# Optimization experiments

Hardware: AMD Instinct MI355X
Metric: run time of the kernel (lower is better)

## Reference

```python
import jax, jax.numpy as jnp
import numpy as np

D_MODEL = 1024
N_HEADS = 16
D_K = D_MODEL // N_HEADS


def _xavier(key, shape):
    fan_in, fan_out = shape[1], shape[0]
    a = np.sqrt(6.0 / (fan_in + fan_out))
    return jax.random.uniform(key, shape, jnp.float32, -a, a)


def setup_inputs() -> dict:
    key = jax.random.key(0)
    kx, kq, kk, kv, ko = jax.random.split(key, 5)
    x = jax.random.normal(kx, (2, 2048, D_MODEL), jnp.float32)
    # nn.Linear weights are [out, in]; y = x @ W.T
    Wq = _xavier(kq, (D_MODEL, D_MODEL))
    Wk = _xavier(kk, (D_MODEL, D_MODEL))
    Wv = _xavier(kv, (D_MODEL, D_MODEL))
    Wo = _xavier(ko, (D_MODEL, D_MODEL))
    bo = jnp.zeros((D_MODEL,), jnp.float32)
    return {"x": x, "Wq": Wq, "Wk": Wk, "Wv": Wv, "Wo": Wo, "bo": bo}


def reference(x, Wq, Wk, Wv, Wo, bo):
    B, S, D = x.shape
    def split_heads(t):
        # [B,S,D] -> [B,H,S,d_k]
        return t.reshape(B, S, N_HEADS, D_K).transpose(0, 2, 1, 3)
    Q = split_heads(x @ Wq.T)
    K = split_heads(x @ Wk.T)
    V = split_heads(x @ Wv.T)
    scale = 1.0 / jnp.sqrt(jnp.asarray(D_K, x.dtype))
    scores = jnp.einsum('bhqd,bhkd->bhqk', Q, K) * scale  # [B,H,S,S]
    attn = jax.nn.softmax(scores, axis=-1)
    out = jnp.einsum('bhqk,bhkd->bhqd', attn, V)  # [B,H,S,d_k]
    out = out.transpose(0, 2, 1, 3).reshape(B, S, D)  # merge heads
    return out @ Wo.T + bo
```

## Files before the change

kernel.cpp:

```cpp
#include <hip/hip_runtime.h>


typedef __attribute__((ext_vector_type(8))) short bf16x8;
typedef __attribute__((ext_vector_type(4))) short bf16x4;
typedef __attribute__((ext_vector_type(4))) float f32x4;
typedef __attribute__((ext_vector_type(2))) unsigned int u32x2;
typedef __attribute__((ext_vector_type(4))) unsigned int u32x4;

#define GK 1024
#define SEQ 2048
#define NHEAD 16
#define DKD 64
#define PADW 72

#define MFMA32(a, b, c) __builtin_amdgcn_mfma_f32_16x16x32_bf16((a), (b), (c), 0, 0, 0)

#if __has_builtin(__builtin_amdgcn_exp2f)
#define EXP2(x) __builtin_amdgcn_exp2f(x)
#else
#define EXP2(x) exp2f(x)
#endif

#define QSCALE 0.18033688011f

static __device__ __forceinline__ unsigned short f2bf(float f) {
    unsigned int u = __float_as_uint(f);
    u += 0x7fffu + ((u >> 16) & 1u);
    return (unsigned short)(u >> 16);
}

static __device__ __forceinline__ unsigned int pack_bf2(float a, float b) {
    unsigned int ua = __float_as_uint(a) + 0x8000u;
    unsigned int ub = __float_as_uint(b) + 0x8000u;
    return __builtin_amdgcn_perm(ub, ua, 0x07060302u);
}

__global__ __launch_bounds__(256) void cast_all(const float* __restrict__ x,
                                                const float* __restrict__ wq,
                                                const float* __restrict__ wk,
                                                const float* __restrict__ wv,
                                                const float* __restrict__ wo,
                                                unsigned short* __restrict__ Xb,
                                                unsigned short* __restrict__ Wqkv,
                                                unsigned short* __restrict__ Wob) {
    const int bid = blockIdx.x;
    const float* src; unsigned short* dst; int off;
    if (bid < 4096)      { src = x;  dst = Xb;             off = bid; }
    else if (bid < 5120) { src = wq; dst = Wqkv;           off = bid - 4096; }
    else if (bid < 6144) { src = wk; dst = Wqkv + 1048576; off = bid - 5120; }
    else if (bid < 7168) { src = wv; dst = Wqkv + 2097152; off = bid - 6144; }
    else                 { src = wo; dst = Wob;            off = bid - 7168; }
    const int i = off * 1024 + threadIdx.x * 4;
    float4 v = *(const float4*)(src + i);
    u32x2 p; p.x = pack_bf2(v.x, v.y); p.y = pack_bf2(v.z, v.w);
    *(u32x2*)(dst + i) = p;
}

template <int MODE, int BN>
__global__ __launch_bounds__(256) void gemm_bt(const unsigned short* __restrict__ A,
                                               const unsigned short* __restrict__ Bw,
                                               unsigned short* __restrict__ outb,
                                               float* __restrict__ outf,
                                               const float* __restrict__ bias) {
    constexpr int NJ = BN / 32;
    constexpr int TILE = (128 + BN) * 32;
    constexpr int LOOP_BYTES = 2 * TILE * 2;
    constexpr int EPI_BYTES  = 4 * 64 * PADW * 2;
    constexpr int SMEM_BYTES = (MODE == 0)
        ? (LOOP_BYTES > EPI_BYTES ? LOOP_BYTES : EPI_BYTES)
        : LOOP_BYTES;
    __shared__ __align__(16) unsigned char SMEM[SMEM_BYTES];
    unsigned short* Buf0 = (unsigned short*)SMEM;
    unsigned short* Buf1 = Buf0 + TILE;

    const int t    = threadIdx.x;
    const int lane = t & 63;
    const int w    = t >> 6;
    const int wm   = (w >> 1) * 64;
    const int wn   = (w & 1) * (BN / 2);
    const int bm0  = blockIdx.x * 128;
    const int bn0  = blockIdx.y * BN;
    const int lm   = lane & 15;
    const int lq   = lane >> 4;
    const int swz  = (lq ^ (lm & 3)) * 8;

    const unsigned short* Ab = A + (size_t)bm0 * GK;
    const unsigned short* Bb = Bw + (size_t)bn0 * GK;

    f32x4 acc[4][NJ];
    const f32x4 Z4 = {0.f, 0.f, 0.f, 0.f};
#pragma unroll
    for (int i = 0; i < 4; i++)
#pragma unroll
        for (int j = 0; j < NJ; j++) acc[i][j] = Z4;

    const int q_uni = (t & ~63);

    auto STAGE = [&](unsigned short* Bp, int k0) {
#pragma unroll
        for (int i = 0; i < 2; ++i) {
            int q  = i * 256 + t;
            int r  = q >> 2;
            int gc = (q & 3) ^ (r & 3);
            int q0 = i * 256 + q_uni;
            __builtin_amdgcn_global_load_lds(
                (const __attribute__((address_space(1))) void*)(Ab + (size_t)r * GK + k0 + gc * 8),
                (__attribute__((address_space(3))) void*)(Bp + (size_t)q0 * 8),
                16, 0, 0);
        }
#pragma unroll
        for (int i = 0; i < BN / 64; ++i) {
            int q  = i * 256 + t;
            int r  = q >> 2;
            int gc = (q & 3) ^ (r & 3);
            int q0 = i * 256 + q_uni;
            __builtin_amdgcn_global_load_lds(
                (const __attribute__((address_space(1))) void*)(Bb + (size_t)r * GK + k0 + gc * 8),
                (__attribute__((address_space(3))) void*)(Bp + 128 * 32 + (size_t)q0 * 8),
                16, 0, 0);
        }
    };

    STAGE(Buf0, 0);
    for (int ks = 0; ks < GK / 32; ++ks) {
        __syncthreads();
        unsigned short* Cur = (ks & 1) ? Buf1 : Buf0;
        unsigned short* Nxt = (ks & 1) ? Buf0 : Buf1;
        if (ks + 1 < GK / 32) STAGE(Nxt, (ks + 1) * 32);

        bf16x8 af[4], bf[NJ];
#pragma unroll
        for (int i = 0; i < 4; i++)
            af[i] = *(const bf16x8*)(Cur + (wm + i * 16 + lm) * 32 + swz);
#pragma unroll
        for (int j = 0; j < NJ; j++)
            bf[j] = *(const bf16x8*)(Cur + 128 * 32 + (wn + j * 16 + lm) * 32 + swz);
#pragma unroll
        for (int i = 0; i < 4; i++)
#pragma unroll
            for (int j = 0; j < NJ; j++)
                acc[i][j] = MFMA32(af[i], bf[j], acc[i][j]);
    }

    if (MODE == 0) {
        __syncthreads();
        unsigned short* E  = (unsigned short*)SMEM;
        unsigned short* Ew = E + w * (64 * PADW);
        const int nbase = bn0 + wn;
        const int which = nbase >> 10;
        const int hh    = (nbase & 1023) >> 6;
        const int lq4   = lq * 4;
        if (which != 2) {
            const float sc = (which == 0) ? QSCALE : 1.0f;
#pragma unroll
            for (int i = 0; i < 4; i++)
#pragma unroll
                for (int j = 0; j < 4; j++)
#pragma unroll
                    for (int r = 0; r < 4; r++)
                        Ew[(i * 16 + lq4 + r) * PADW + j * 16 + lm] =
                            f2bf(acc[i][j][r] * sc);
            unsigned short* dst = outb + (size_t)which * 4194304;
#pragma unroll
            for (int rep = 0; rep < 8; ++rep) {
                const int mm = rep * 8 + (lane >> 3);
                const int d0 = (lane & 7) * 8;
                uint4 v = *(const uint4*)(Ew + mm * PADW + d0);
                const int m_g = bm0 + wm + mm;
                const int b = m_g >> 11, s = m_g & 2047;
                *(uint4*)(dst + (((size_t)(b * NHEAD + hh)) * SEQ + s) * DKD + d0) = v;
            }
        } else {
#pragma unroll
            for (int i = 0; i < 4; i++)
#pragma unroll
                for (int j = 0; j < 4; j++) {
                    u32x2 pk;
                    pk.x = pack_bf2(acc[i][j][0], acc[i][j][1]);
                    pk.y = pack_bf2(acc[i][j][2], acc[i][j][3]);
                    *(u32x2*)(Ew + (j * 16 + lm) * PADW + i * 16 + lq4) = pk;
                }
            unsigned short* dst = outb + (size_t)2 * 4194304;
#pragma unroll
            for (int rep = 0; rep < 8; ++rep) {
                const int nn = rep * 8 + (lane >> 3);
                const int mc = (lane & 7) * 8;
                uint4 v = *(const uint4*)(Ew + nn * PADW + mc);
                const int m_g = bm0 + wm + mc;
                const int b = m_g >> 11, s0 = m_g & 2047;
                *(uint4*)(dst + (((size_t)(b * NHEAD + hh)) * DKD + nn) * SEQ + s0) = v;
            }
        }
    } else {
#pragma unroll
        for (int i = 0; i < 4; i++) {
            const int mbase = bm0 + wm + i * 16 + lq * 4;
#pragma unroll
            for (int j = 0; j < NJ; j++) {
                const int n = bn0 + wn + j * 16 + lm;
#pragma unroll
                for (int r = 0; r < 4; r++)
                    outf[(size_t)(mbase + r) * 1024 + n] = acc[i][j][r] + bias[n];
            }
        }
    }
}

__global__ __launch_bounds__(256, 2) void attn_kernel(const unsigned short* __restrict__ Qg,
                                                      const unsigned short* __restrict__ Kg,
                                                      const unsigned short* __restrict__ Vtg,
                                                      unsigned short* __restrict__ Og) {
    __shared__ __align__(16) unsigned short KV[2][2][64 * PADW];

    const int id  = blockIdx.x;
    const int xcd = id & 7;
    const int j8  = id >> 3;
    const int bh  = xcd * 4 + (j8 & 3);
    const int qb  = j8 >> 2;
    const unsigned short* Qp  = Qg  + ((size_t)bh * SEQ + qb * 128) * DKD;
    const unsigned short* Kp  = Kg  + (size_t)bh * SEQ * DKD;
    const unsigned short* Vtp = Vtg + (size_t)bh * DKD * SEQ;

    const int t    = threadIdx.x;
    const int lane = t & 63;
    const int w    = t >> 6;
    const int qg   = w >> 1;
    const int kg   = w & 1;
    const int lm   = lane & 15;
    const int kq   = lane >> 4;

    const f32x4 Z4 = {0.f, 0.f, 0.f, 0.f};

    bf16x8 aq[2][2][2];
#pragma unroll
    for (int h2 = 0; h2 < 2; ++h2)
#pragma unroll
        for (int c = 0; c < 2; ++c)
#pragma unroll
            for (int kk = 0; kk < 2; ++kk)
                aq[h2][c][kk] = *(const bf16x8*)(Qp + (size_t)(h2 * 64 + qg * 32 + c * 16 + lm) * DKD + kk * 32 + kq * 8);

    f32x4 o[2][2][4];
    float ls[2][2];
#pragma unroll
    for (int h2 = 0; h2 < 2; ++h2)
#pragma unroll
        for (int c = 0; c < 2; ++c) {
            ls[h2][c] = 0.f;
#pragma unroll
            for (int dj = 0; dj < 4; ++dj) o[h2][c][dj] = Z4;
        }

    const int sr = t >> 2, sc = (t & 3) * 16;
    uint4 kreg0, kreg1, vreg0, vreg1;
    {
        const unsigned short* kp = Kp + (size_t)sr * DKD + sc;
        const unsigned short* vp = Vtp + (size_t)sr * SEQ + sc;
        uint4 a0 = *(const uint4*)(kp), a1 = *(const uint4*)(kp + 8);
        uint4 b0 = *(const uint4*)(vp), b1 = *(const uint4*)(vp + 8);
        uint4* dk = (uint4*)(&KV[0][0][sr * PADW + sc]); dk[0] = a0; dk[1] = a1;
        uint4* dv = (uint4*)(&KV[0][1][sr * PADW + sc]); dv[0] = b0; dv[1] = b1;
    }
    {
        const unsigned short* kp = Kp + (size_t)(64 + sr) * DKD + sc;
        kreg0 = *(const uint4*)(kp); kreg1 = *(const uint4*)(kp + 8);
        const unsigned short* vp = Vtp + (size_t)sr * SEQ + 64 + sc;
        vreg0 = *(const uint4*)(vp); vreg1 = *(const uint4*)(vp + 8);
    }

    for (int kt = 0; kt < 32; ++kt) {
        asm volatile("s_waitcnt lgkmcnt(0)\n\ts_barrier" ::: "memory");
        const unsigned short* Kc = &KV[kt & 1][0][0];
        const unsigned short* Vc = &KV[kt & 1][1][0];

        bf16x8 ak[2][2];
#pragma unroll
        for (int kc = 0; kc < 2; ++kc)
#pragma unroll
            for (int kk = 0; kk < 2; ++kk)
                ak[kc][kk] = *(const bf16x8*)(Kc + (kg * 32 + kc * 16 + lm) * PADW + kk * 32 + kq * 8);

        if (kt + 1 < 32) {
            uint4* dk = (uint4*)(&KV[(kt + 1) & 1][0][sr * PADW + sc]);
            dk[0] = kreg0; dk[1] = kreg1;
            uint4* dv = (uint4*)(&KV[(kt + 1) & 1][1][sr * PADW + sc]);
            dv[0] = vreg0; dv[1] = vreg1;
        }
        if (kt + 2 < 32) {
            const unsigned short* kp = Kp + (size_t)((kt + 2) * 64 + sr) * DKD + sc;
            kreg0 = *(const uint4*)(kp); kreg1 = *(const uint4*)(kp + 8);
            const unsigned short* vp = Vtp + (size_t)sr * SEQ + (kt + 2) * 64 + sc;
            vreg0 = *(const uint4*)(vp); vreg1 = *(const uint4*)(vp + 8);
        }

        bf16x8 bv[4];
#pragma unroll
        for (int dj = 0; dj < 4; ++dj) {
            const unsigned short* vr = Vc + (dj * 16 + lm) * PADW + kg * 32;
            u32x2 lo = __builtin_bit_cast(u32x2, *(const bf16x4*)(vr + kq * 4));
            u32x2 hi = __builtin_bit_cast(u32x2, *(const bf16x4*)(vr + 16 + kq * 4));
            u32x4 uu; uu.x = lo.x; uu.y = lo.y; uu.z = hi.x; uu.w = hi.y;
            bv[dj] = __builtin_bit_cast(bf16x8, uu);
        }

#pragma unroll
        for (int h2 = 0; h2 < 2; ++h2) {
            f32x4 s[2][2];
            __builtin_amdgcn_s_setprio(1);
#pragma unroll
            for (int kc = 0; kc < 2; ++kc)
#pragma unroll
                for (int c = 0; c < 2; ++c) {
                    s[kc][c] = MFMA32(ak[kc][0], aq[h2][c][0], Z4);
                    s[kc][c] = MFMA32(ak[kc][1], aq[h2][c][1], s[kc][c]);
                }
            __builtin_amdgcn_s_setprio(0);

#pragma unroll
            for (int c = 0; c < 2; ++c) {
#pragma unroll
                for (int kc = 0; kc < 2; ++kc)
#pragma unroll
                    for (int r = 0; r < 4; ++r) s[kc][c][r] = EXP2(s[kc][c][r]);
                ls[h2][c] += ((s[0][c][0] + s[0][c][1]) + (s[0][c][2] + s[0][c][3]))
                           + ((s[1][c][0] + s[1][c][1]) + (s[1][c][2] + s[1][c][3]));
            }

            bf16x8 pa[2];
#pragma unroll
            for (int c = 0; c < 2; ++c) {
                u32x4 uu;
                uu.x = pack_bf2(s[0][c][0], s[0][c][1]);
                uu.y = pack_bf2(s[0][c][2], s[0][c][3]);
                uu.z = pack_bf2(s[1][c][0], s[1][c][1]);
                uu.w = pack_bf2(s[1][c][2], s[1][c][3]);
                pa[c] = __builtin_bit_cast(bf16x8, uu);
            }

            __builtin_amdgcn_s_setprio(1);
#pragma unroll
            for (int dj = 0; dj < 4; ++dj)
#pragma unroll
                for (int c = 0; c < 2; ++c)
                    o[h2][c][dj] = MFMA32(pa[c], bv[dj], o[h2][c][dj]);
            __builtin_amdgcn_s_setprio(0);
        }
    }

    __syncthreads();
    float* Lf = (float*)(&KV[0][0][0]);

#pragma unroll
    for (int h2 = 0; h2 < 2; ++h2)
#pragma unroll
        for (int c = 0; c < 2; ++c) {
            float v = ls[h2][c];
            v += __shfl_xor(v, 16);
            v += __shfl_xor(v, 32);
            if (kq == 0) Lf[(h2 * 4 + w) * 32 + c * 16 + lm] = v;
        }
    __syncthreads();

    const int rq = t >> 2;
    const int dq = (t & 3) * 8;
    const int qgr = rq >> 5, qlr = rq & 31;
    float li[2];
#pragma unroll
    for (int h2 = 0; h2 < 2; ++h2) {
        float l = Lf[(h2 * 4 + qgr * 2) * 32 + qlr] + Lf[(h2 * 4 + qgr * 2 + 1) * 32 + qlr];
#if __has_builtin(__builtin_amdgcn_rcpf)
        li[h2] = __builtin_amdgcn_rcpf(l);
#else
        li[h2] = 1.0f / l;
#endif
    }
    __syncthreads();

    const int b = bh >> 4, h = bh & 15;
#pragma unroll
    for (int p = 0; p < 2; ++p) {
#pragma unroll
        for (int h2 = 0; h2 < 2; ++h2)
#pragma unroll
            for (int c = 0; c < 2; ++c)
#pragma unroll
                for (int djh = 0; djh < 2; ++djh) {
                    const int dj = 2 * p + djh;
#pragma unroll
                    for (int r = 0; r < 4; ++r)
                        Lf[((h2 * 4 + w) * 32 + c * 16 + kq * 4 + r) * 36 + djh * 16 + lm] = o[h2][c][dj][r];
                }
        __syncthreads();
#pragma unroll
        for (int h2 = 0; h2 < 2; ++h2) {
            const int rowA = ((h2 * 4 + qgr * 2) * 32 + qlr) * 36;
            const int rowB = ((h2 * 4 + qgr * 2 + 1) * 32 + qlr) * 36;
            f32x4 a0 = *(const f32x4*)(Lf + rowA + dq) + *(const f32x4*)(Lf + rowB + dq);
            f32x4 a1 = *(const f32x4*)(Lf + rowA + dq + 4) + *(const f32x4*)(Lf + rowB + dq + 4);
            uint4 outv;
            outv.x = pack_bf2(a0[0] * li[h2], a0[1] * li[h2]);
            outv.y = pack_bf2(a0[2] * li[h2], a0[3] * li[h2]);
            outv.z = pack_bf2(a1[0] * li[h2], a1[1] * li[h2]);
            outv.w = pack_bf2(a1[2] * li[h2], a1[3] * li[h2]);
            *(uint4*)(Og + (((size_t)(b * SEQ + qb * 128 + h2 * 64 + rq)) * NHEAD + h) * DKD + p * 32 + dq) = outv;
        }
        __syncthreads();
    }
}

extern "C" void kernel_launch(void* const* d_in, const int* in_sizes, int n_in,
                              void* d_out, int out_size, void* d_ws, size_t ws_size,
                              hipStream_t stream) {
    const float* x  = (const float*)d_in[0];
    const float* Wq = (const float*)d_in[1];
    const float* Wk = (const float*)d_in[2];
    const float* Wv = (const float*)d_in[3];
    const float* Wo = (const float*)d_in[4];
    const float* bo = (const float*)d_in[5];
    float* out = (float*)d_out;

    unsigned short* ws = (unsigned short*)d_ws;
    unsigned short* Xb   = ws;
    unsigned short* Wqkv = ws + 4194304;
    unsigned short* Wob  = ws + 7340032;
    unsigned short* QKV  = ws + 8388608;
    unsigned short* Ob   = ws + 20971520;

    cast_all<<<8192, 256, 0, stream>>>(x, Wq, Wk, Wv, Wo, Xb, Wqkv, Wob);
    gemm_bt<0, 128><<<dim3(32, 24), 256, 0, stream>>>(Xb, Wqkv, QKV, nullptr, nullptr);
    attn_kernel<<<512, 256, 0, stream>>>(QKV, QKV + 4194304, QKV + 8388608, Ob);
    gemm_bt<1, 64><<<dim3(32, 16), 256, 0, stream>>>(Ob, Wob, nullptr, out, bo);
}
```

Before: 176.9 us.

## Split attention key range across two wave groups per block

The attention block doubles to 512 threads. Two groups of four waves each process half of the 2048-key sequence with separate double-buffered K/V tiles, and the partial row sums and outputs are combined through shared memory at the end. The aim is more waves in flight and a shorter serial loop per block (16 tiles instead of 32), so latency hides better. In exchange it costs more LDS per block, doubles the launch-bounds occupancy target (which tightens the per-thread register budget), and adds a larger reduction epilogue. The final stores also narrow to 8-byte writes.

Measured after the change: 363.3 us. +105.4%, slower.

```diff
diff --git a/kernel.cpp b/kernel.cpp
--- a/kernel.cpp
+++ b/kernel.cpp
@@ -206,11 +206,11 @@
     }
 }
 
-__global__ __launch_bounds__(256, 2) void attn_kernel(const unsigned short* __restrict__ Qg,
+__global__ __launch_bounds__(512, 4) void attn_kernel(const unsigned short* __restrict__ Qg,
                                                       const unsigned short* __restrict__ Kg,
                                                       const unsigned short* __restrict__ Vtg,
                                                       unsigned short* __restrict__ Og) {
-    __shared__ __align__(16) unsigned short KV[2][2][64 * PADW];
+    __shared__ __align__(16) unsigned short KV[2][2][2][64 * PADW];
 
     const int id  = blockIdx.x;
     const int xcd = id & 7;
@@ -224,7 +224,8 @@
     const int t    = threadIdx.x;
     const int lane = t & 63;
     const int w    = t >> 6;
-    const int qg   = w >> 1;
+    const int sg   = w >> 2;
+    const int qg   = (w & 3) >> 1;
     const int kg   = w & 1;
     const int lm   = lane & 15;
     const int kq   = lane >> 4;
@@ -251,27 +252,26 @@
             for (int dj = 0; dj < 4; ++dj) o[h2][c][dj] = Z4;
         }
 
-    const int sr = t >> 2, sc = (t & 3) * 16;
+    const int tl = t & 255;
+    const int sr = tl >> 2, sc = (tl & 3) * 16;
+    const unsigned short* KpW = Kp + (size_t)(sg * 1024 + sr) * DKD + sc;
+    const unsigned short* VpW = Vtp + (size_t)sr * SEQ + sg * 1024 + sc;
     uint4 kreg0, kreg1, vreg0, vreg1;
     {
-        const unsigned short* kp = Kp + (size_t)sr * DKD + sc;
-        const unsigned short* vp = Vtp + (size_t)sr * SEQ + sc;
-        uint4 a0 = *(const uint4*)(kp), a1 = *(const uint4*)(kp + 8);
-        uint4 b0 = *(const uint4*)(vp), b1 = *(const uint4*)(vp + 8);
-        uint4* dk = (uint4*)(&KV[0][0][sr * PADW + sc]); dk[0] = a0; dk[1] = a1;
-        uint4* dv = (uint4*)(&KV[0][1][sr * PADW + sc]); dv[0] = b0; dv[1] = b1;
+        uint4 a0 = *(const uint4*)(KpW), a1 = *(const uint4*)(KpW + 8);
+        uint4 b0 = *(const uint4*)(VpW), b1 = *(const uint4*)(VpW + 8);
+        uint4* dk = (uint4*)(&KV[sg][0][0][sr * PADW + sc]); dk[0] = a0; dk[1] = a1;
+        uint4* dv = (uint4*)(&KV[sg][0][1][sr * PADW + sc]); dv[0] = b0; dv[1] = b1;
     }
     {
-        const unsigned short* kp = Kp + (size_t)(64 + sr) * DKD + sc;
-        kreg0 = *(const uint4*)(kp); kreg1 = *(const uint4*)(kp + 8);
-        const unsigned short* vp = Vtp + (size_t)sr * SEQ + 64 + sc;
-        vreg0 = *(const uint4*)(vp); vreg1 = *(const uint4*)(vp + 8);
-    }
-
-    for (int kt = 0; kt < 32; ++kt) {
+        kreg0 = *(const uint4*)(KpW + 64 * DKD); kreg1 = *(const uint4*)(KpW + 64 * DKD + 8);
+        vreg0 = *(const uint4*)(VpW + 64);       vreg1 = *(const uint4*)(VpW + 64 + 8);
+    }
+
+    for (int kt = 0; kt < 16; ++kt) {
         asm volatile("s_waitcnt lgkmcnt(0)\n\ts_barrier" ::: "memory");
-        const unsigned short* Kc = &KV[kt & 1][0][0];
-        const unsigned short* Vc = &KV[kt & 1][1][0];
+        const unsigned short* Kc = &KV[sg][kt & 1][0][0];
+        const unsigned short* Vc = &KV[sg][kt & 1][1][0];
 
         bf16x8 ak[2][2];
 #pragma unroll
@@ -280,16 +280,16 @@
             for (int kk = 0; kk < 2; ++kk)
                 ak[kc][kk] = *(const bf16x8*)(Kc + (kg * 32 + kc * 16 + lm) * PADW + kk * 32 + kq * 8);
 
-        if (kt + 1 < 32) {
-            uint4* dk = (uint4*)(&KV[(kt + 1) & 1][0][sr * PADW + sc]);
+        if (kt + 1 < 16) {
+            uint4* dk = (uint4*)(&KV[sg][(kt + 1) & 1][0][sr * PADW + sc]);
             dk[0] = kreg0; dk[1] = kreg1;
-            uint4* dv = (uint4*)(&KV[(kt + 1) & 1][1][sr * PADW + sc]);
+            uint4* dv = (uint4*)(&KV[sg][(kt + 1) & 1][1][sr * PADW + sc]);
             dv[0] = vreg0; dv[1] = vreg1;
         }
-        if (kt + 2 < 32) {
-            const unsigned short* kp = Kp + (size_t)((kt + 2) * 64 + sr) * DKD + sc;
+        if (kt + 2 < 16) {
+            const unsigned short* kp = KpW + (size_t)(kt + 2) * 64 * DKD;
             kreg0 = *(const uint4*)(kp); kreg1 = *(const uint4*)(kp + 8);
-            const unsigned short* vp = Vtp + (size_t)sr * SEQ + (kt + 2) * 64 + sc;
+            const unsigned short* vp = VpW + (kt + 2) * 64;
             vreg0 = *(const uint4*)(vp); vreg1 = *(const uint4*)(vp + 8);
         }
 
@@ -348,7 +348,7 @@
     }
 
     __syncthreads();
-    float* Lf = (float*)(&KV[0][0][0]);
+    float* Lf = (float*)(&KV[0][0][0][0]);
 
 #pragma unroll
     for (int h2 = 0; h2 < 2; ++h2)
@@ -357,17 +357,19 @@
             float v = ls[h2][c];
             v += __shfl_xor(v, 16);
             v += __shfl_xor(v, 32);
-            if (kq == 0) Lf[(h2 * 4 + w) * 32 + c * 16 + lm] = v;
+            if (kq == 0) Lf[(h2 * 8 + w) * 32 + c * 16 + lm] = v;
         }
     __syncthreads();
 
-    const int rq = t >> 2;
-    const int dq = (t & 3) * 8;
+    const int rq  = t >> 3;
+    const int dq  = (t & 7) * 4;
     const int qgr = rq >> 5, qlr = rq & 31;
+    const int w0  = qgr * 2;
     float li[2];
 #pragma unroll
     for (int h2 = 0; h2 < 2; ++h2) {
-        float l = Lf[(h2 * 4 + qgr * 2) * 32 + qlr] + Lf[(h2 * 4 + qgr * 2 + 1) * 32 + qlr];
+        float l = (Lf[(h2 * 8 + w0) * 32 + qlr]     + Lf[(h2 * 8 + w0 + 1) * 32 + qlr])
+                + (Lf[(h2 * 8 + w0 + 4) * 32 + qlr] + Lf[(h2 * 8 + w0 + 5) * 32 + qlr]);
 #if __has_builtin(__builtin_amdgcn_rcpf)
         li[h2] = __builtin_amdgcn_rcpf(l);
 #else
@@ -388,21 +390,19 @@
                     const int dj = 2 * p + djh;
 #pragma unroll
                     for (int r = 0; r < 4; ++r)
-                        Lf[((h2 * 4 + w) * 32 + c * 16 + kq * 4 + r) * 36 + djh * 16 + lm] = o[h2][c][dj][r];
+                        Lf[((h2 * 8 + w) * 32 + c * 16 + kq * 4 + r) * 36 + djh * 16 + lm] = o[h2][c][dj][r];
                 }
         __syncthreads();
 #pragma unroll
         for (int h2 = 0; h2 < 2; ++h2) {
-            const int rowA = ((h2 * 4 + qgr * 2) * 32 + qlr) * 36;
-            const int rowB = ((h2 * 4 + qgr * 2 + 1) * 32 + qlr) * 36;
-            f32x4 a0 = *(const f32x4*)(Lf + rowA + dq) + *(const f32x4*)(Lf + rowB + dq);
-            f32x4 a1 = *(const f32x4*)(Lf + rowA + dq + 4) + *(const f32x4*)(Lf + rowB + dq + 4);
-            uint4 outv;
-            outv.x = pack_bf2(a0[0] * li[h2], a0[1] * li[h2]);
-            outv.y = pack_bf2(a0[2] * li[h2], a0[3] * li[h2]);
-            outv.z = pack_bf2(a1[0] * li[h2], a1[1] * li[h2]);
-            outv.w = pack_bf2(a1[2] * li[h2], a1[3] * li[h2]);
-            *(uint4*)(Og + (((size_t)(b * SEQ + qb * 128 + h2 * 64 + rq)) * NHEAD + h) * DKD + p * 32 + dq) = outv;
+            f32x4 a = *(const f32x4*)(Lf + ((h2 * 8 + w0) * 32 + qlr) * 36 + dq)
+                    + *(const f32x4*)(Lf + ((h2 * 8 + w0 + 1) * 32 + qlr) * 36 + dq)
+                    + *(const f32x4*)(Lf + ((h2 * 8 + w0 + 4) * 32 + qlr) * 36 + dq)
+                    + *(const f32x4*)(Lf + ((h2 * 8 + w0 + 5) * 32 + qlr) * 36 + dq);
+            u32x2 outv;
+            outv.x = pack_bf2(a[0] * li[h2], a[1] * li[h2]);
+            outv.y = pack_bf2(a[2] * li[h2], a[3] * li[h2]);
+            *(u32x2*)(Og + (((size_t)(b * SEQ + qb * 128 + h2 * 64 + rq)) * NHEAD + h) * DKD + p * 32 + dq) = outv;
         }
         __syncthreads();
     }
@@ -428,6 +428,6 @@
 
     cast_all<<<8192, 256, 0, stream>>>(x, Wq, Wk, Wv, Wo, Xb, Wqkv, Wob);
     gemm_bt<0, 128><<<dim3(32, 24), 256, 0, stream>>>(Xb, Wqkv, QKV, nullptr, nullptr);
-    attn_kernel<<<512, 256, 0, stream>>>(QKV, QKV + 4194304, QKV + 8388608, Ob);
+    attn_kernel<<<512, 512, 0, stream>>>(QKV, QKV + 4194304, QKV + 8388608, Ob);
     gemm_bt<1, 64><<<dim3(32, 16), 256, 0, stream>>>(Ob, Wob, nullptr, out, bo);
 }
```

## Remap GEMM workgroups across XCDs and add BK=64 output projection kernel

Applied to the files above, without the earlier changes.

Adds an XCD-aware block index remap so consecutive tiles of the same column block land on the same XCD, improving L2 reuse in both GEMMs. Replaces the output projection with a dedicated kernel that stages 64-wide K slices (half as many iterations and barriers) with an XOR-swizzled LDS layout. This uses more LDS per block, which may reduce occupancy.

Result: no change. 176.5 us (-0.2%).

```diff
diff --git a/kernel.cpp b/kernel.cpp
--- a/kernel.cpp
+++ b/kernel.cpp
@@ -33,6 +33,11 @@
     unsigned int ua = __float_as_uint(a) + 0x8000u;
     unsigned int ub = __float_as_uint(b) + 0x8000u;
     return __builtin_amdgcn_perm(ub, ua, 0x07060302u);
+}
+
+static __device__ __forceinline__ int xcd_remap(int nwg) {
+    const int lid = blockIdx.x + 32 * blockIdx.y;
+    return (lid & 7) * (nwg >> 3) + (lid >> 3);
 }
 
 __global__ __launch_bounds__(256) void cast_all(const float* __restrict__ x,
@@ -78,8 +83,9 @@
     const int w    = t >> 6;
     const int wm   = (w >> 1) * 64;
     const int wn   = (w & 1) * (BN / 2);
-    const int bm0  = blockIdx.x * 128;
-    const int bn0  = blockIdx.y * BN;
+    const int sid  = xcd_remap(32 * gridDim.y);
+    const int bm0  = (sid & 31) * 128;
+    const int bn0  = (sid >> 5) * BN;
     const int lm   = lane & 15;
     const int lq   = lane >> 4;
     const int swz  = (lq ^ (lm & 3)) * 8;
@@ -202,6 +208,101 @@
                 for (int r = 0; r < 4; r++)
                     outf[(size_t)(mbase + r) * 1024 + n] = acc[i][j][r] + bias[n];
             }
+        }
+    }
+}
+
+__global__ __launch_bounds__(256) void gemm_out(const unsigned short* __restrict__ A,
+                                                const unsigned short* __restrict__ Bw,
+                                                float* __restrict__ outf,
+                                                const float* __restrict__ bias) {
+    constexpr int BN = 64;
+    constexpr int TILE = (128 + BN) * 64;
+    __shared__ __align__(16) unsigned short Buf[2 * TILE];
+
+    const int t    = threadIdx.x;
+    const int lane = t & 63;
+    const int w    = t >> 6;
+    const int wm   = (w >> 1) * 64;
+    const int wn   = (w & 1) * 32;
+    const int sid  = xcd_remap(32 * gridDim.y);
+    const int bm0  = (sid & 31) * 128;
+    const int bn0  = (sid >> 5) * BN;
+    const int lm   = lane & 15;
+    const int lq   = lane >> 4;
+    const int swzb = lm & 7;
+
+    const unsigned short* Ab = A + (size_t)bm0 * GK;
+    const unsigned short* Bb = Bw + (size_t)bn0 * GK;
+
+    f32x4 acc[4][2];
+    const f32x4 Z4 = {0.f, 0.f, 0.f, 0.f};
+#pragma unroll
+    for (int i = 0; i < 4; i++)
+#pragma unroll
+        for (int j = 0; j < 2; j++) acc[i][j] = Z4;
+
+    const int q_uni = (t & ~63);
+
+    auto STAGE = [&](unsigned short* Bp, int k0) {
+#pragma unroll
+        for (int i = 0; i < 4; ++i) {
+            int q  = i * 256 + t;
+            int r  = q >> 3;
+            int gc = (q & 7) ^ (r & 7);
+            int q0 = i * 256 + q_uni;
+            __builtin_amdgcn_global_load_lds(
+                (const __attribute__((address_space(1))) void*)(Ab + (size_t)r * GK + k0 + gc * 8),
+                (__attribute__((address_space(3))) void*)(Bp + (size_t)q0 * 8),
+                16, 0, 0);
+        }
+#pragma unroll
+        for (int i = 0; i < 2; ++i) {
+            int q  = i * 256 + t;
+            int r  = q >> 3;
+            int gc = (q & 7) ^ (r & 7);
+            int q0 = i * 256 + q_uni;
+            __builtin_amdgcn_global_load_lds(
+                (const __attribute__((address_space(1))) void*)(Bb + (size_t)r * GK + k0 + gc * 8),
+                (__attribute__((address_space(3))) void*)(Bp + 128 * 64 + (size_t)q0 * 8),
+                16, 0, 0);
+        }
+    };
+
+    STAGE(Buf, 0);
+    for (int ks = 0; ks < GK / 64; ++ks) {
+        __syncthreads();
+        unsigned short* Cur = Buf + (ks & 1) * TILE;
+        unsigned short* Nxt = Buf + ((ks & 1) ^ 1) * TILE;
+        if (ks + 1 < GK / 64) STAGE(Nxt, (ks + 1) * 64);
+
+#pragma unroll
+        for (int kk = 0; kk < 2; ++kk) {
+            const int swz = ((kk * 4 + lq) ^ swzb) * 8;
+            bf16x8 af[4], bf[2];
+#pragma unroll
+            for (int i = 0; i < 4; i++)
+                af[i] = *(const bf16x8*)(Cur + (wm + i * 16 + lm) * 64 + swz);
+#pragma unroll
+            for (int j = 0; j < 2; j++)
+                bf[j] = *(const bf16x8*)(Cur + 128 * 64 + (wn + j * 16 + lm) * 64 + swz);
+#pragma unroll
+            for (int i = 0; i < 4; i++)
+#pragma unroll
+                for (int j = 0; j < 2; j++)
+                    acc[i][j] = MFMA32(af[i], bf[j], acc[i][j]);
+        }
+    }
+
+#pragma unroll
+    for (int i = 0; i < 4; i++) {
+        const int mbase = bm0 + wm + i * 16 + lq * 4;
+#pragma unroll
+        for (int j = 0; j < 2; j++) {
+            const int n = bn0 + wn + j * 16 + lm;
+#pragma unroll
+            for (int r = 0; r < 4; r++)
+                outf[(size_t)(mbase + r) * 1024 + n] = acc[i][j][r] + bias[n];
         }
     }
 }
@@ -429,5 +530,5 @@
     cast_all<<<8192, 256, 0, stream>>>(x, Wq, Wk, Wv, Wo, Xb, Wqkv, Wob);
     gemm_bt<0, 128><<<dim3(32, 24), 256, 0, stream>>>(Xb, Wqkv, QKV, nullptr, nullptr);
     attn_kernel<<<512, 256, 0, stream>>>(QKV, QKV + 4194304, QKV + 8388608, Ob);
-    gemm_bt<1, 64><<<dim3(32, 16), 256, 0, stream>>>(Ob, Wob, nullptr, out, bo);
-}
+    gemm_out<<<dim3(32, 16), 256, 0, stream>>>(Ob, Wob, out, bo);
+}
```
